# Performance work log

Hardware: AMD Instinct MI355X
Metric: run time of the kernel (lower is better)

The kernel has to match this reference:

```python
import jax, jax.numpy as jnp
import numpy as np

N, IN_DIM = 50000, 1024
E = 100000
NUM_REL = 40
HEADS, OUT_DIM = 4, 200
HID = HEADS * OUT_DIM  # 800
B = 8192
NEG_SLOPE = 0.2


def setup_inputs() -> dict:
    key = jax.random.key(0)
    ks = jax.random.split(key, 12)
    node_emb = jax.random.normal(ks[0], (N, IN_DIM), dtype=jnp.float32)
    # RelGAT learnable params
    W = jax.random.normal(ks[1], (IN_DIM, HID), dtype=jnp.float32) * (1.0 / np.sqrt(IN_DIM))
    bias = jnp.zeros((HID,), dtype=jnp.float32)
    a_src = jax.random.normal(ks[2], (HEADS, OUT_DIM), dtype=jnp.float32) * 0.1
    a_dst = jax.random.normal(ks[3], (HEADS, OUT_DIM), dtype=jnp.float32) * 0.1
    a_rel = jax.random.normal(ks[4], (HEADS, OUT_DIM), dtype=jnp.float32) * 0.1
    rel_feat = jax.random.normal(ks[5], (NUM_REL, HID), dtype=jnp.float32) * 0.1
    # DistMult scorer relation embeddings
    rel_emb = jax.random.normal(ks[6], (NUM_REL, HID), dtype=jnp.float32) * 0.1
    # Graph structure (constants)
    edge_index = jax.random.randint(ks[7], (2, E), 0, N, dtype=jnp.int64)
    edge_type = jax.random.randint(ks[8], (E,), 0, NUM_REL, dtype=jnp.int64)
    # Triple batch
    src_ids = jax.random.randint(ks[9], (B,), 0, N, dtype=jnp.int64)
    rel_ids = jax.random.randint(ks[10], (B,), 0, NUM_REL, dtype=jnp.int64)
    dst_ids = jax.random.randint(ks[11], (B,), 0, N, dtype=jnp.int64)
    return dict(node_emb=node_emb, W=W, bias=bias, a_src=a_src, a_dst=a_dst,
                a_rel=a_rel, rel_feat=rel_feat, rel_emb=rel_emb,
                edge_index=edge_index, edge_type=edge_type,
                src_ids=src_ids, rel_ids=rel_ids, dst_ids=dst_ids)


def _rel_gat(node_emb, W, bias, a_src, a_dst, a_rel, rel_feat, edge_index, edge_type):
    src, dst = edge_index[0], edge_index[1]
    h = (node_emb @ W).reshape(N, HEADS, OUT_DIM)          # [N,H,D]
    hs = h[src]                                            # [E,H,D] gather
    hd = h[dst]                                            # [E,H,D] gather
    r = rel_feat[edge_type].reshape(E, HEADS, OUT_DIM)     # [E,H,D]
    # relation-conditioned attention logits per head
    logits = (jnp.einsum('ehd,hd->eh', hs, a_src)
              + jnp.einsum('ehd,hd->eh', hd, a_dst)
              + jnp.einsum('ehd,hd->eh', r, a_rel))        # [E,H]
    logits = jax.nn.leaky_relu(logits, NEG_SLOPE)
    # segment softmax over incoming edges of each destination node
    seg_max = jax.ops.segment_max(logits, dst, num_segments=N)   # [N,H]
    e = jnp.exp(logits - seg_max[dst])                           # [E,H]
    denom = jax.ops.segment_sum(e, dst, num_segments=N)          # [N,H]
    alpha = e / denom[dst]                                       # [E,H]
    # weighted scatter-aggregate of source messages
    out = jax.ops.segment_sum(alpha[:, :, None] * hs, dst, num_segments=N)  # [N,H,D]
    return out.reshape(N, HID) + bias                            # dropout: eval mode (identity)


def reference(node_emb, W, bias, a_src, a_dst, a_rel, rel_feat, rel_emb,
              edge_index, edge_type, src_ids, rel_ids, dst_ids):
    refined = _rel_gat(node_emb, W, bias, a_src, a_dst, a_rel, rel_feat,
                       edge_index, edge_type)                # [N, HID]
    src_vec = refined[src_ids]                               # [B, HID]
    dst_vec = refined[dst_ids]                               # [B, HID]
    # DistMult: sum(s * r * d)
    scores = jnp.sum(src_vec * rel_emb[rel_ids] * dst_vec, axis=-1)  # [B]
    return scores
```

## Files before the change

### kernel.cpp

```cpp
#include <hip/hip_runtime.h>
#include <hip/hip_bf16.h>
#include <math.h>

#define NN 50000
#define IN_DIM 1024
#define EE 100000
#define NUM_REL 40
#define HEADS 4
#define OUT_D 200
#define HID 800
#define BB 8192
#define SLOT_CAP 16384
#define SRC_CAP 50176
#define WT_COLS 896

typedef __attribute__((ext_vector_type(8))) short short8;
typedef __attribute__((ext_vector_type(4))) float f32x4;

__device__ inline unsigned short f2bf(float f) {
    unsigned int u = __float_as_uint(f);
    u += 0x7FFF + ((u >> 16) & 1);
    return (unsigned short)(u >> 16);
}
__device__ inline float bf2f(unsigned short s) {
    return __uint_as_float(((unsigned int)s) << 16);
}
__device__ inline void gl2lds16(const unsigned short* g, unsigned short* l) {
    __builtin_amdgcn_global_load_lds(
        (const __attribute__((address_space(1))) void*)g,
        (__attribute__((address_space(3))) void*)l, 16, 0, 0);
}
__device__ inline short8 cvt8(float4 u, float4 v) {
    union { unsigned int w[4]; short8 s; } r;
    asm("v_cvt_pk_bf16_f32 %0, %1, %2" : "=v"(r.w[0]) : "v"(u.x), "v"(u.y));
    asm("v_cvt_pk_bf16_f32 %0, %1, %2" : "=v"(r.w[1]) : "v"(u.z), "v"(u.w));
    asm("v_cvt_pk_bf16_f32 %0, %1, %2" : "=v"(r.w[2]) : "v"(v.x), "v"(v.y));
    asm("v_cvt_pk_bf16_f32 %0, %1, %2" : "=v"(r.w[3]) : "v"(v.z), "v"(v.w));
    return r.s;
}

__device__ inline int wave_compact(bool won, int* ctr) {
    unsigned long long m = __ballot(won);
    if (!m) return -1;
    int lane = threadIdx.x & 63;
    int leader = __ffsll((long long)m) - 1;
    int base = 0;
    if (lane == leader) base = atomicAdd(ctr, __popcll(m));
    base = __shfl(base, leader, 64);
    return won ? base + __popcll(m & ((1ull << lane) - 1)) : -1;
}

#define INIT_BLOCKS 196
__global__ __launch_bounds__(256) void k_init_wa(int* slot_of_node, int* xrow_of_node,
                                                 int* deg, int* counters,
                                                 const float* W, const float* a_src,
                                                 const float* a_dst, const float* a_rel,
                                                 const float* rel_feat, float* Wa, float* prel) {
    int b = blockIdx.x;
    if (b < INIT_BLOCKS) {
        int i = b * 256 + threadIdx.x;
        if (i < NN) { slot_of_node[i] = -1; xrow_of_node[i] = -1; }
        if (i < SLOT_CAP) deg[i] = 0;
        if (i < 8) counters[i] = 0;
        return;
    }
    int wid = (b - INIT_BLOCKS) * 4 + (threadIdx.x >> 6);
    int lane = threadIdx.x & 63;
    if (wid >= IN_DIM * 8 + NUM_REL * HEADS) return;
    float acc = 0.f;
    int d = lane * 4;
    if (d < OUT_D) {
        const float* row;
        const float* a;
        if (wid < IN_DIM * 8) {
            int k = wid >> 3, c = wid & 7;
            int h = c & 3;
            row = W + (size_t)k * HID + h * OUT_D;
            a = ((c < 4) ? a_src : a_dst) + h * OUT_D;
        } else {
            int j = wid - IN_DIM * 8;
            int r = j >> 2, h = j & 3;
            row = rel_feat + (size_t)r * HID + h * OUT_D;
            a = a_rel + h * OUT_D;
        }
        float4 wv = *(const float4*)(row + d);
        float4 av = *(const float4*)(a + d);
        acc = wv.x * av.x + wv.y * av.y + wv.z * av.z + wv.w * av.w;
    }
    for (int off = 32; off; off >>= 1) acc += __shfl_down(acc, off, 64);
    if (lane == 0) {
        if (wid < IN_DIM * 8) Wa[wid] = acc;
        else prel[wid - IN_DIM * 8] = acc;
    }
}

__global__ void k_build_slots(const int* src_ids, const int* dst_ids,
                              int* slot_of_node, int* counters, int* scorelist) {
    int i = blockIdx.x * 256 + threadIdx.x;
    bool valid = i < 2 * BB;
    int n = 0;
    bool won = false;
    if (valid) {
        n = (i < BB) ? src_ids[i] : dst_ids[i - BB];
        if (slot_of_node[n] == -1)
            won = (atomicCAS(&slot_of_node[n], -1, -2) == -1);
    }
    int s = wave_compact(won, &counters[0]);
    if (won) {
        slot_of_node[n] = s;
        scorelist[s] = n;
    }
}

__global__ void k_edge0(const int* ei, const int* slot_of_node,
                        int* xrow_of_node, int* counters, int* rows, int* deg) {
    int e = blockIdx.x * 256 + threadIdx.x;
    bool valid = e < EE;
    int slot = -1, sn = 0;
    if (valid) {
        int dn = ei[EE + e];
        slot = slot_of_node[dn];
    }
    bool surv = valid && slot >= 0;
    bool won = false;
    if (surv) {
        sn = ei[e];
        if (xrow_of_node[sn] == -1)
            won = (atomicCAS(&xrow_of_node[sn], -1, -2) == -1);
    }
    int t = wave_compact(won, &counters[1]);
    if (won) {
        rows[t] = sn;
        xrow_of_node[sn] = t;
    }
    if (surv) atomicAdd(&deg[slot], 1);
}

__global__ __launch_bounds__(256) void k_tail_scan_wt(const int* scorelist, int* xrow_of_node,
                                                      int* counters, int* rows,
                                                      const int* deg, int* base, int* cursor,
                                                      const float* W, const float* Wa,
                                                      unsigned short* Wt) {
    int t = threadIdx.x;
    if (blockIdx.x == 0) {
        __shared__ int pref[257];
        int s = 0;
        const int4* dv = (const int4*)(deg + t * (SLOT_CAP / 256));
        for (int i = 0; i < SLOT_CAP / 256 / 4; ++i) {
            int4 v = dv[i];
            s += v.x + v.y + v.z + v.w;
        }
        pref[t + 1] = s;
        if (t == 0) pref[0] = 0;
        __syncthreads();
        if (t == 0)
            for (int i = 1; i <= 256; ++i) pref[i] += pref[i - 1];
        __syncthreads();
        int r = pref[t];
        for (int i = 0; i < SLOT_CAP / 256; ++i) {
            int idx = t * (SLOT_CAP / 256) + i;
            base[idx] = r;
            cursor[idx] = r;
            r += deg[idx];
        }
        return;
    }
    if (blockIdx.x <= 64) {
        int i = (blockIdx.x - 1) * 256 + t;
        bool valid = i < counters[0];
        int n = 0;
        bool won = false;
        if (valid) {
            n = scorelist[i];
            won = (xrow_of_node[n] < 0);
        }
        int tt = wave_compact(won, &counters[3]);
        if (won) {
            int xr = counters[1] + tt;
            xrow_of_node[n] = xr;
            rows[xr] = n;
        }
        return;
    }
    __shared__ float tile[64][65];
    int b = blockIdx.x - 65;
    int k0 = (b & 15) * 64, c0 = (b >> 4) * 64;
    {
        int kk = t >> 2, cc = (t & 3) * 16;
        for (int i = 0; i < 16; ++i) {
            int c = c0 + cc + i;
            float v = 0.f;
            if (c < HID) v = W[(size_t)(k0 + kk) * HID + c];
            else if (c < HID + 8) v = Wa[(size_t)(k0 + kk) * 8 + (c - HID)];
            tile[cc + i][kk] = v;
        }
    }
    __syncthreads();
    {
        int cc = t >> 2, kk = (t & 3) * 16;
        unsigned short o[16];
        for (int i = 0; i < 16; ++i) o[i] = f2bf(tile[cc][kk + i]);
        *(short8*)(Wt + (size_t)(c0 + cc) * IN_DIM + k0 + kk) = *(short8*)o;
        *(short8*)(Wt + (size_t)(c0 + cc) * IN_DIM + k0 + kk + 8) = *(short8*)(o + 8);
    }
}

#define GBM 128
#define GBN 128
#define GBK 32

#define ALOADR(K) do {                                                  \
    const float* p0 = ax0 + (size_t)(K) * 32;                           \
    const float* p1 = ax1 + (size_t)(K) * 32;                           \
    av0 = *(const float4*)(p0);                                         \
    av1 = *(const float4*)(p0 + 4);                                     \
    av2 = *(const float4*)(p1);                                         \
    av3 = *(const float4*)(p1 + 4);                                     \
} while (0)

#define AWRITE(AS) do {                                                 \
    short8 s0 = cvt8(av0, av1);                                         \
    short8 s1 = cvt8(av2, av3);                                         \
    *(short8*)&(AS)[(size_t)t * 8] = s0;                                \
    *(short8*)&(AS)[(size_t)(256 + t) * 8] = s1;                        \
} while (0)

#define BSTAGE(BS, K) do {                                              \
    gl2lds16(bP0 + (size_t)(K) * 32, (BS) + (size_t)t * 8);             \
    gl2lds16(bP1 + (size_t)(K) * 32, (BS) + (size_t)(256 + t) * 8);     \
} while (0)

#define COMPUTE(AS, BS) do {                                            \
    short8 af[4], bf4[4];                                               \
    _Pragma("unroll")                                                   \
    for (int i = 0; i < 4; ++i)                                         \
        af[i] = *(const short8*)&(AS)[(size_t)((ga + i) * 64 + lane) * 8]; \
    _Pragma("unroll")                                                   \
    for (int j = 0; j < 4; ++j)                                         \
        bf4[j] = *(const short8*)&(BS)[(size_t)((gb + j) * 64 + lane) * 8]; \
    __builtin_amdgcn_s_setprio(1);                                      \
    _Pragma("unroll")                                                   \
    for (int i = 0; i < 4; ++i)                                         \
        _Pragma("unroll")                                               \
        for (int j = 0; j < 4; ++j)                                     \
            acc[i][j] = __builtin_amdgcn_mfma_f32_16x16x32_bf16(af[i], bf4[j], acc[i][j], 0, 0, 0); \
    __builtin_amdgcn_s_setprio(0);                                      \
} while (0)

#define GATE asm volatile("s_waitcnt vmcnt(0) lgkmcnt(0)\n\ts_barrier" ::: "memory")

__global__ __launch_bounds__(256, 3) void k_hgemm(const float* x, const int* rows,
                                                  const unsigned short* Wt,
                                                  const int* counters, unsigned short* h_src,
                                                  float* sS, float* sD) {
    int nsrc = counters[1];
    int nneed = nsrc + counters[3];
    int lin = blockIdx.x + 7 * blockIdx.y;
    int g = lin / 56, r = lin % 56;
    int rowb = g * 8 + (r & 7);
    int colb = r >> 3;
    int col0 = colb * GBN;
    int row0 = rowb * GBM;
    int rowlim = (col0 == 768) ? nneed : nsrc;
    if (row0 >= rowlim) return;
    __shared__ unsigned short As0[GBM * GBK];
    __shared__ unsigned short As1[GBM * GBK];
    __shared__ unsigned short Bs0[GBN * GBK];
    __shared__ unsigned short Bs1[GBN * GBK];
    int t = threadIdx.x;
    int r0 = ((t >> 6) << 4) + (t & 15);
    int ko = ((t >> 4) & 3) << 3;
    int lim = nneed - 1;
    int n0 = rows[min(row0 + r0, lim)];
    int n1 = rows[min(row0 + r0 + 64, lim)];
    const float* ax0 = x + (size_t)n0 * IN_DIM + ko;
    const float* ax1 = x + (size_t)n1 * IN_DIM + ko;
    const unsigned short* bP0 = Wt + (size_t)(col0 + r0) * IN_DIM + ko;
    const unsigned short* bP1 = bP0 + (size_t)64 * IN_DIM;
    int w = t >> 6, lane = t & 63;
    int ga = (w >> 1) * 4, gb = (w & 1) * 4;
    int wr = (w >> 1) * 64, wc = (w & 1) * 64;
    int fm = lane & 15, fq = lane >> 4;
    float4 av0, av1, av2, av3;
    f32x4 acc[4][4] = {};
    ALOADR(0);
    BSTAGE(Bs0, 0);
    AWRITE(As0);
    GATE;
#pragma unroll 1
    for (int k = 0; k < 32; k += 2) {
        ALOADR(k + 1);
        BSTAGE(Bs1, k + 1);
        COMPUTE(As0, Bs0);
        AWRITE(As1);
        GATE;
        if (k < 30) {
            ALOADR(k + 2);
            BSTAGE(Bs0, k + 2);
        }
        COMPUTE(As1, Bs1);
        if (k < 30) {
            AWRITE(As0);
            GATE;
        }
    }
#pragma unroll
    for (int i = 0; i < 4; ++i) {
#pragma unroll
        for (int j = 0; j < 4; ++j) {
            int gcol = col0 + wc + j * 16 + fm;
            if (gcol >= HID + 8) continue;
#pragma unroll
            for (int rr = 0; rr < 4; ++rr) {
                int grow = row0 + wr + i * 16 + fq * 4 + rr;
                float v = acc[i][j][rr];
                if (gcol < HID) {
                    if (grow < nsrc) h_src[(size_t)grow * HID + gcol] = f2bf(v);
                } else if (grow < nneed) {
                    int c = gcol - HID;
                    if (c < 4) sS[grow * 4 + c] = v;
                    else sD[grow * 4 + (c - 4)] = v;
                }
            }
        }
    }
}

__global__ void k_place(const int* ei, const int* etype, const int* slot_of_node,
                        const int* xrow_of_node, int* cursor,
                        const float* sS, const float* sD, const float* prel,
                        float* clogit, int* tlist) {
    int e = blockIdx.x * 256 + threadIdx.x;
    if (e >= EE) return;
    int dn = ei[EE + e];
    int slot = slot_of_node[dn];
    if (slot < 0) return;
    int sn = ei[e];
    int r = etype[e];
    int xs = xrow_of_node[sn];
    int xd = xrow_of_node[dn];
    int pos = atomicAdd(&cursor[slot], 1);
    tlist[pos] = xs;
    float4 lg;
    float* lp = (float*)&lg;
#pragma unroll
    for (int h = 0; h < 4; ++h) {
        float v = sS[xs * 4 + h] + sD[xd * 4 + h] + prel[r * 4 + h];
        lp[h] = v > 0.f ? v : 0.2f * v;
    }
    *(float4*)&clogit[(size_t)pos * 4] = lg;
}

__global__ __launch_bounds__(256) void k_aggregate(const int* counters, const int* base,
                                                   const int* deg, const int* tlist,
                                                   const float* clogit,
                                                   const unsigned short* h_src, const float* bias,
                                                   float* refined) {
    int b = blockIdx.x;
    if (b >= counters[0]) return;
    int beg = base[b], d = deg[b];
    __shared__ float m4[4], den4[4];
    __shared__ float alpha[64][4];
    __shared__ int tsl[64];
    int t = threadIdx.x;
    if (t < 4) {
        float m = -3e38f;
        for (int j = 0; j < d; ++j)
            m = fmaxf(m, clogit[(size_t)(beg + j) * 4 + t]);
        float s = 0.f;
        for (int j = 0; j < d; ++j)
            s += expf(clogit[(size_t)(beg + j) * 4 + t] - m);
        m4[t] = m;
        den4[t] = s;
    }
    __syncthreads();
    int head = t / 50;
    float4 acc = {0.f, 0.f, 0.f, 0.f};
    for (int j0 = 0; j0 < d; j0 += 64) {
        int nc = min(64, d - j0);
        if (t < nc * 4) {
            int j = t >> 2, h = t & 3;
            alpha[j][h] = expf(clogit[(size_t)(beg + j0 + j) * 4 + h] - m4[h]) / den4[h];
            if (h == 0) tsl[j] = tlist[beg + j0 + j];
        }
        __syncthreads();
        if (t < 200) {
            for (int j = 0; j < nc; ++j) {
                float a = alpha[j][head];
                ushort4 hv = *(const ushort4*)(h_src + (size_t)tsl[j] * HID + t * 4);
                acc.x += a * bf2f(hv.x);
                acc.y += a * bf2f(hv.y);
                acc.z += a * bf2f(hv.z);
                acc.w += a * bf2f(hv.w);
            }
        }
        __syncthreads();
    }
    if (t < 200) {
        float4 bv = *(const float4*)(bias + t * 4);
        float4 o = {acc.x + bv.x, acc.y + bv.y, acc.z + bv.z, acc.w + bv.w};
        *(float4*)(refined + (size_t)b * HID + t * 4) = o;
    }
}

__global__ __launch_bounds__(256) void k_score(const int* src_ids, const int* rel_ids,
                                               const int* dst_ids, const int* slot_of_node,
                                               const float* rel_emb, const float* refined,
                                               float* out) {
    int gid = blockIdx.x * 256 + threadIdx.x;
    int b = gid >> 6;
    int lane = threadIdx.x & 63;
    if (b >= BB) return;
    int ss = slot_of_node[src_ids[b]];
    int ds = slot_of_node[dst_ids[b]];
    int r = rel_ids[b];
    const float* sv = refined + (size_t)ss * HID;
    const float* dv = refined + (size_t)ds * HID;
    const float* rv = rel_emb + (size_t)r * HID;
    float acc = 0.f;
    for (int c4 = lane; c4 < 200; c4 += 64) {
        float4 s = *(const float4*)(sv + c4 * 4);
        float4 dq = *(const float4*)(dv + c4 * 4);
        float4 rr = *(const float4*)(rv + c4 * 4);
        acc += s.x * rr.x * dq.x + s.y * rr.y * dq.y + s.z * rr.z * dq.z + s.w * rr.w * dq.w;
    }
    for (int off = 32; off; off >>= 1) acc += __shfl_down(acc, off, 64);
    if (lane == 0) out[b] = acc;
}

extern "C" void kernel_launch(void* const* d_in, const int* in_sizes, int n_in,
                              void* d_out, int out_size, void* d_ws, size_t ws_size,
                              hipStream_t stream) {
    const float* node_emb = (const float*)d_in[0];
    const float* W        = (const float*)d_in[1];
    const float* bias     = (const float*)d_in[2];
    const float* a_src    = (const float*)d_in[3];
    const float* a_dst    = (const float*)d_in[4];
    const float* a_rel    = (const float*)d_in[5];
    const float* rel_feat = (const float*)d_in[6];
    const float* rel_emb  = (const float*)d_in[7];
    const int* edge_index = (const int*)d_in[8];
    const int* edge_type  = (const int*)d_in[9];
    const int* src_ids    = (const int*)d_in[10];
    const int* rel_ids    = (const int*)d_in[11];
    const int* dst_ids    = (const int*)d_in[12];
    float* out = (float*)d_out;

    char* w = (char*)d_ws;
    auto alloc = [&](size_t bytes) -> void* {
        void* p = (void*)w;
        w += (bytes + 255) & ~(size_t)255;
        return p;
    };
    int* slot_of_node = (int*)alloc((size_t)NN * 4);
    int* xrow_of_node = (int*)alloc((size_t)NN * 4);
    int* scorelist    = (int*)alloc((size_t)SLOT_CAP * 4);
    int* rows         = (int*)alloc((size_t)NN * 4);
    int* counters     = (int*)alloc(256);
    int* deg          = (int*)alloc((size_t)SLOT_CAP * 4);
    int* base         = (int*)alloc((size_t)SLOT_CAP * 4);
    int* cursor       = (int*)alloc((size_t)SLOT_CAP * 4);
    int* tlist        = (int*)alloc((size_t)EE * 4);
    float* clogit = (float*)alloc((size_t)EE * 4 * 4);
    float* sS     = (float*)alloc((size_t)SRC_CAP * 4 * 4);
    float* sD     = (float*)alloc((size_t)SRC_CAP * 4 * 4);
    float* Wa     = (float*)alloc((size_t)IN_DIM * 8 * 4);
    float* prel   = (float*)alloc((size_t)NUM_REL * 4 * 4);
    unsigned short* Wt    = (unsigned short*)alloc((size_t)WT_COLS * IN_DIM * 2);
    unsigned short* h_src = (unsigned short*)alloc((size_t)SRC_CAP * HID * 2);
    float* refined = (float*)alloc((size_t)SLOT_CAP * HID * 4);

    int wa_blocks = (IN_DIM * 8 + NUM_REL * HEADS + 3) / 4;
    k_init_wa<<<INIT_BLOCKS + wa_blocks, 256, 0, stream>>>(
        slot_of_node, xrow_of_node, deg, counters,
        W, a_src, a_dst, a_rel, rel_feat, Wa, prel);
    k_build_slots<<<(2 * BB + 255) / 256, 256, 0, stream>>>(src_ids, dst_ids, slot_of_node,
                                                            counters, scorelist);
    k_edge0<<<(EE + 255) / 256, 256, 0, stream>>>(edge_index, slot_of_node,
                                                  xrow_of_node, counters, rows, deg);
    k_tail_scan_wt<<<65 + 224, 256, 0, stream>>>(scorelist, xrow_of_node, counters,
                                                 rows, deg, base, cursor, W, Wa, Wt);
    dim3 ggrid(7, 392);
    k_hgemm<<<ggrid, 256, 0, stream>>>(node_emb, rows, Wt, counters, h_src, sS, sD);
    k_place<<<(EE + 255) / 256, 256, 0, stream>>>(edge_index, edge_type, slot_of_node,
                                                  xrow_of_node, cursor, sS, sD, prel,
                                                  clogit, tlist);
    k_aggregate<<<SLOT_CAP, 256, 0, stream>>>(counters, base, deg, tlist,
                                              clogit, h_src, bias, refined);
    k_score<<<(BB * 64 + 255) / 256, 256, 0, stream>>>(src_ids, rel_ids, dst_ids,
                                                       slot_of_node, rel_emb, refined, out);
}
```

Before: 492.1 us.

## Pre-tile weights into MFMA fragment order and triple-buffer B staging in GEMM

The weight transpose kernel now writes W into a blocked layout matching the GEMM's LDS fragment order, so each B stage is one contiguous 8KB chunk. The GEMM A-load is reorganized so each thread reads contiguous 16-byte float4 rows (8 threads per row) and writes 4-element bf16 pieces into fragment positions. The main loop moves from double-buffered B with full vmcnt(0) waits to triple-buffered B with a vmcnt(2) wait, which keeps the next B stage in flight across the barrier. The cost is extra LDS and more complex per-thread addressing. The transpose kernel also loses its LDS tile and now does strided global reads of W.

```diff
diff --git a/kernel.cpp b/kernel.cpp
--- a/kernel.cpp
+++ b/kernel.cpp
@@ -12,10 +12,10 @@
 #define BB 8192
 #define SLOT_CAP 16384
 #define SRC_CAP 50176
-#define WT_COLS 896
 
 typedef __attribute__((ext_vector_type(8))) short short8;
 typedef __attribute__((ext_vector_type(4))) float f32x4;
+typedef __attribute__((ext_vector_type(2))) unsigned int u32x2;
 
 __device__ inline unsigned short f2bf(float f) {
     unsigned int u = __float_as_uint(f);
@@ -30,13 +30,11 @@
         (const __attribute__((address_space(1))) void*)g,
         (__attribute__((address_space(3))) void*)l, 16, 0, 0);
 }
-__device__ inline short8 cvt8(float4 u, float4 v) {
-    union { unsigned int w[4]; short8 s; } r;
-    asm("v_cvt_pk_bf16_f32 %0, %1, %2" : "=v"(r.w[0]) : "v"(u.x), "v"(u.y));
-    asm("v_cvt_pk_bf16_f32 %0, %1, %2" : "=v"(r.w[1]) : "v"(u.z), "v"(u.w));
-    asm("v_cvt_pk_bf16_f32 %0, %1, %2" : "=v"(r.w[2]) : "v"(v.x), "v"(v.y));
-    asm("v_cvt_pk_bf16_f32 %0, %1, %2" : "=v"(r.w[3]) : "v"(v.z), "v"(v.w));
-    return r.s;
+__device__ inline u32x2 cvt4(float4 v) {
+    u32x2 r;
+    asm("v_cvt_pk_bf16_f32 %0, %1, %2" : "=v"(r.x) : "v"(v.x), "v"(v.y));
+    asm("v_cvt_pk_bf16_f32 %0, %1, %2" : "=v"(r.y) : "v"(v.z), "v"(v.w));
+    return r;
 }
 
 __device__ inline int wave_compact(bool won, int* ctr) {
@@ -182,52 +180,51 @@
         }
         return;
     }
-    __shared__ float tile[64][65];
-    int b = blockIdx.x - 65;
-    int k0 = (b & 15) * 64, c0 = (b >> 4) * 64;
-    {
-        int kk = t >> 2, cc = (t & 3) * 16;
-        for (int i = 0; i < 16; ++i) {
-            int c = c0 + cc + i;
-            float v = 0.f;
-            if (c < HID) v = W[(size_t)(k0 + kk) * HID + c];
-            else if (c < HID + 8) v = Wa[(size_t)(k0 + kk) * 8 + (c - HID)];
-            tile[cc + i][kk] = v;
-        }
-    }
-    __syncthreads();
-    {
-        int cc = t >> 2, kk = (t & 3) * 16;
-        unsigned short o[16];
-        for (int i = 0; i < 16; ++i) o[i] = f2bf(tile[cc][kk + i]);
-        *(short8*)(Wt + (size_t)(c0 + cc) * IN_DIM + k0 + kk) = *(short8*)o;
-        *(short8*)(Wt + (size_t)(c0 + cc) * IN_DIM + k0 + kk + 8) = *(short8*)(o + 8);
+    int bw = blockIdx.x - 65;
+    int n0 = bw >> 5, ks = bw & 31;
+    unsigned short* dst = Wt + (size_t)(n0 * 32 + ks) * 512 * 8;
+#pragma unroll
+    for (int q = 0; q < 2; ++q) {
+        int c = q * 256 + t;
+        int col = ((c >> 6) << 4) + (c & 15);
+        int kc = (c >> 4) & 3;
+        int gcol = n0 * 128 + col;
+        int kbase = ks * 32 + kc * 8;
+        unsigned short o[8];
+        if (gcol < HID) {
+#pragma unroll
+            for (int kj = 0; kj < 8; ++kj) o[kj] = f2bf(W[(size_t)(kbase + kj) * HID + gcol]);
+        } else if (gcol < HID + 8) {
+#pragma unroll
+            for (int kj = 0; kj < 8; ++kj) o[kj] = f2bf(Wa[(size_t)(kbase + kj) * 8 + (gcol - HID)]);
+        } else {
+#pragma unroll
+            for (int kj = 0; kj < 8; ++kj) o[kj] = 0;
+        }
+        *(short8*)(dst + (size_t)c * 8) = *(short8*)o;
     }
 }
 
 #define GBM 128
 #define GBN 128
-#define GBK 32
 
 #define ALOADR(K) do {                                                  \
-    const float* p0 = ax0 + (size_t)(K) * 32;                           \
-    const float* p1 = ax1 + (size_t)(K) * 32;                           \
-    av0 = *(const float4*)(p0);                                         \
-    av1 = *(const float4*)(p0 + 4);                                     \
-    av2 = *(const float4*)(p1);                                         \
-    av3 = *(const float4*)(p1 + 4);                                     \
+    avA0 = *(const float4*)(ax0 + (size_t)(K) * 32);                    \
+    avA1 = *(const float4*)(ax1 + (size_t)(K) * 32);                    \
+    avA2 = *(const float4*)(ax2 + (size_t)(K) * 32);                    \
+    avA3 = *(const float4*)(ax3 + (size_t)(K) * 32);                    \
 } while (0)
 
 #define AWRITE(AS) do {                                                 \
-    short8 s0 = cvt8(av0, av1);                                         \
-    short8 s1 = cvt8(av2, av3);                                         \
-    *(short8*)&(AS)[(size_t)t * 8] = s0;                                \
-    *(short8*)&(AS)[(size_t)(256 + t) * 8] = s1;                        \
+    *(u32x2*)((AS) + acw)        = cvt4(avA0);                          \
+    *(u32x2*)((AS) + acw + 1024) = cvt4(avA1);                          \
+    *(u32x2*)((AS) + acw + 2048) = cvt4(avA2);                          \
+    *(u32x2*)((AS) + acw + 3072) = cvt4(avA3);                          \
 } while (0)
 
-#define BSTAGE(BS, K) do {                                              \
-    gl2lds16(bP0 + (size_t)(K) * 32, (BS) + (size_t)t * 8);             \
-    gl2lds16(bP1 + (size_t)(K) * 32, (BS) + (size_t)(256 + t) * 8);     \
+#define BSTAGE(BS, KS) do {                                             \
+    gl2lds16(bsrc + ((size_t)(KS) * 512 + t) * 8,       (BS) + (size_t)t * 8);       \
+    gl2lds16(bsrc + ((size_t)(KS) * 512 + 256 + t) * 8, (BS) + (size_t)(256 + t) * 8); \
 } while (0)
 
 #define COMPUTE(AS, BS) do {                                            \
@@ -247,7 +244,9 @@
     __builtin_amdgcn_s_setprio(0);                                      \
 } while (0)
 
-#define GATE asm volatile("s_waitcnt vmcnt(0) lgkmcnt(0)\n\ts_barrier" ::: "memory")
+#define WAIT2   asm volatile("s_waitcnt vmcnt(2)" ::: "memory")
+#define WAIT0   asm volatile("s_waitcnt vmcnt(0)" ::: "memory")
+#define PUBBAR  asm volatile("s_waitcnt lgkmcnt(0)\n\ts_barrier" ::: "memory")
 
 __global__ __launch_bounds__(256, 3) void k_hgemm(const float* x, const int* rows,
                                                   const unsigned short* Wt,
@@ -261,49 +260,52 @@
     int colb = r >> 3;
     int col0 = colb * GBN;
     int row0 = rowb * GBM;
-    int rowlim = (col0 == 768) ? nneed : nsrc;
+    int rowlim = (colb == 6) ? nneed : nsrc;
     if (row0 >= rowlim) return;
-    __shared__ unsigned short As0[GBM * GBK];
-    __shared__ unsigned short As1[GBM * GBK];
-    __shared__ unsigned short Bs0[GBN * GBK];
-    __shared__ unsigned short Bs1[GBN * GBK];
+    __shared__ unsigned short As0[4096], As1[4096];
+    __shared__ unsigned short Bs0[4096], Bs1[4096], Bs2[4096];
     int t = threadIdx.x;
-    int r0 = ((t >> 6) << 4) + (t & 15);
-    int ko = ((t >> 4) & 3) << 3;
+    int r0 = t >> 3;
+    int fo = (t & 7) * 4;
     int lim = nneed - 1;
-    int n0 = rows[min(row0 + r0, lim)];
-    int n1 = rows[min(row0 + r0 + 64, lim)];
-    const float* ax0 = x + (size_t)n0 * IN_DIM + ko;
-    const float* ax1 = x + (size_t)n1 * IN_DIM + ko;
-    const unsigned short* bP0 = Wt + (size_t)(col0 + r0) * IN_DIM + ko;
-    const unsigned short* bP1 = bP0 + (size_t)64 * IN_DIM;
+    const float* ax0 = x + (size_t)rows[min(row0 + r0,      lim)] * IN_DIM + fo;
+    const float* ax1 = x + (size_t)rows[min(row0 + r0 + 32, lim)] * IN_DIM + fo;
+    const float* ax2 = x + (size_t)rows[min(row0 + r0 + 64, lim)] * IN_DIM + fo;
+    const float* ax3 = x + (size_t)rows[min(row0 + r0 + 96, lim)] * IN_DIM + fo;
+    int kc = (t & 7) >> 1, half = t & 1;
+    int acw = (((r0 >> 4) * 64) + kc * 16 + (r0 & 15)) * 8 + half * 4;
+    const unsigned short* bsrc = Wt + (size_t)colb * 32 * 512 * 8;
     int w = t >> 6, lane = t & 63;
     int ga = (w >> 1) * 4, gb = (w & 1) * 4;
     int wr = (w >> 1) * 64, wc = (w & 1) * 64;
     int fm = lane & 15, fq = lane >> 4;
-    float4 av0, av1, av2, av3;
+    float4 avA0, avA1, avA2, avA3;
     f32x4 acc[4][4] = {};
+    unsigned short *bA = Bs0, *bB = Bs1, *bC = Bs2;
+    unsigned short *aC = As0, *aW = As1;
+    BSTAGE(bA, 0);
     ALOADR(0);
-    BSTAGE(Bs0, 0);
-    AWRITE(As0);
-    GATE;
+    BSTAGE(bB, 1);
+    WAIT2;
+    AWRITE(aC);
+    ALOADR(1);
+    PUBBAR;
 #pragma unroll 1
-    for (int k = 0; k < 32; k += 2) {
-        ALOADR(k + 1);
-        BSTAGE(Bs1, k + 1);
-        COMPUTE(As0, Bs0);
-        AWRITE(As1);
-        GATE;
-        if (k < 30) {
-            ALOADR(k + 2);
-            BSTAGE(Bs0, k + 2);
-        }
-        COMPUTE(As1, Bs1);
-        if (k < 30) {
-            AWRITE(As0);
-            GATE;
-        }
-    }
+    for (int k = 0; k < 30; ++k) {
+        BSTAGE(bC, k + 2);
+        COMPUTE(aC, bA);
+        WAIT2;
+        AWRITE(aW);
+        ALOADR(k + 2);
+        PUBBAR;
+        unsigned short* tb = bA; bA = bB; bB = bC; bC = tb;
+        unsigned short* ta = aC; aC = aW; aW = ta;
+    }
+    COMPUTE(aC, bA);
+    WAIT0;
+    AWRITE(aW);
+    PUBBAR;
+    COMPUTE(aW, bB);
 #pragma unroll
     for (int i = 0; i < 4; ++i) {
 #pragma unroll
@@ -466,7 +468,7 @@
     float* sD     = (float*)alloc((size_t)SRC_CAP * 4 * 4);
     float* Wa     = (float*)alloc((size_t)IN_DIM * 8 * 4);
     float* prel   = (float*)alloc((size_t)NUM_REL * 4 * 4);
-    unsigned short* Wt    = (unsigned short*)alloc((size_t)WT_COLS * IN_DIM * 2);
+    unsigned short* Wt    = (unsigned short*)alloc((size_t)7 * 32 * 512 * 8 * 2);
     unsigned short* h_src = (unsigned short*)alloc((size_t)SRC_CAP * HID * 2);
     float* refined = (float*)alloc((size_t)SLOT_CAP * HID * 4);
 
```

Result: faster. 461.0 us (-6.3%).
